# Optimization experiments

Measured on AMD Instinct MI355X. Metric: run time of the kernel, lower is better.

Reference implementation:

```python
import jax, jax.numpy as jnp
import numpy as np

N_ROWS = 262144
FEAT = 1024
N_CORES = 4096
SEG = N_ROWS // N_CORES
H1 = H2 = H3 = 1024
NUM_CLASSES = 2
BN_EPS = 1e-5


def setup_inputs() -> dict:
    key = jax.random.key(0)
    ks = jax.random.split(key, 12)
    x = jax.random.normal(ks[0], (N_ROWS, FEAT), dtype=jnp.float32)
    # equal-length segments: start indices 0, SEG, 2*SEG, ...
    corelen = (jnp.arange(N_CORES) * SEG).astype(jnp.int64)
    def lin(k, din, dout):
        kw, kb = jax.random.split(k)
        W = jax.random.normal(kw, (din, dout), dtype=jnp.float32) / np.sqrt(din)
        b = jnp.zeros((dout,), dtype=jnp.float32)
        return W, b
    W1, b1 = lin(ks[1], FEAT, H1)
    W2, b2 = lin(ks[2], H1, H2)
    W3, b3 = lin(ks[3], H2, H3)
    W4, b4 = lin(ks[4], H3, NUM_CLASSES)
    g1 = jnp.ones((H1,), jnp.float32); be1 = jnp.zeros((H1,), jnp.float32)
    g2 = jnp.ones((H2,), jnp.float32); be2 = jnp.zeros((H2,), jnp.float32)
    g3 = jnp.ones((H3,), jnp.float32); be3 = jnp.zeros((H3,), jnp.float32)
    return {"x": x, "corelen": corelen,
            "W1": W1, "b1": b1, "g1": g1, "be1": be1,
            "W2": W2, "b2": b2, "g2": g2, "be2": be2,
            "W3": W3, "b3": b3, "g3": g3, "be3": be3,
            "W4": W4, "b4": b4}


def _batchnorm(h, g, b):
    # BatchNorm1d, training mode: biased batch statistics over the batch dim
    m = jnp.mean(h, axis=0)
    v = jnp.mean(jnp.square(h - m), axis=0)
    return g * (h - m) * jax.lax.rsqrt(v + BN_EPS) + b


def reference(x, corelen, W1, b1, g1, be1, W2, b2, g2, be2, W3, b3, g3, be3, W4, b4):
    n = x.shape[0]
    # segment id of row r = number of starts <= r, minus 1 (rows before
    # corelen[0] get id -1 and are dropped, matching the torch loop)
    seg_ids = jnp.searchsorted(corelen, jnp.arange(n), side="right") - 1
    agg = jax.ops.segment_sum(x, seg_ids, num_segments=corelen.shape[0])  # [C, FEAT]
    h = jax.nn.relu(_batchnorm(agg @ W1 + b1, g1, be1))
    h = jax.nn.relu(_batchnorm(h @ W2 + b2, g2, be2))
    h = jax.nn.relu(_batchnorm(h @ W3 + b3, g3, be3))
    return h @ W4 + b4  # [C, NUM_CLASSES]
```

## Files before the change

### kernel.cpp

```cpp
#include <hip/hip_runtime.h>
#include <hip/hip_bf16.h>
#include <stdint.h>

#define N_ROWS 262144
#define FEAT 1024
#define N_CORES 4096
#define HDIM 1024
#define BN_EPS 1e-5f

typedef __attribute__((ext_vector_type(8))) short bf16x8;
typedef __attribute__((ext_vector_type(8))) unsigned short u16x8;
typedef __attribute__((ext_vector_type(4))) float f32x4;

__device__ __forceinline__ unsigned short f2bf(float f) {
  __hip_bfloat16 h = __float2bfloat16(f);
  return __builtin_bit_cast(unsigned short, h);
}
__device__ __forceinline__ float bf2f(unsigned short u) {
  unsigned int x = ((unsigned int)u) << 16;
  return __builtin_bit_cast(float, x);
}

__device__ __forceinline__ void gll16(const unsigned short* g, unsigned short* l) {
  __builtin_amdgcn_global_load_lds(
      (const __attribute__((address_space(1))) void*)g,
      (__attribute__((address_space(3))) void*)l, 16, 0, 0);
}

__global__ __launch_bounds__(256)
void k_segsum(const float* __restrict__ x, const int* __restrict__ corelen,
              unsigned short* __restrict__ aggb) {
  const int seg = blockIdx.x;
  const int t = threadIdx.x;
  const int start = corelen[seg];
  const int end = (seg + 1 < N_CORES) ? corelen[seg + 1] : N_ROWS;
  float4 a0 = make_float4(0.f, 0.f, 0.f, 0.f);
  float4 a1 = make_float4(0.f, 0.f, 0.f, 0.f);
  const float* xp = x + (size_t)start * FEAT + t * 4;
  int r = start;
  for (; r + 2 <= end; r += 2) {
    const float4 v0 = *(const float4*)xp;
    const float4 v1 = *(const float4*)(xp + FEAT);
    a0.x += v0.x; a0.y += v0.y; a0.z += v0.z; a0.w += v0.w;
    a1.x += v1.x; a1.y += v1.y; a1.z += v1.z; a1.w += v1.w;
    xp += 2 * FEAT;
  }
  if (r < end) {
    const float4 v0 = *(const float4*)xp;
    a0.x += v0.x; a0.y += v0.y; a0.z += v0.z; a0.w += v0.w;
  }
  a0.x += a1.x; a0.y += a1.y; a0.z += a1.z; a0.w += a1.w;
  ushort4 o;
  o.x = f2bf(a0.x); o.y = f2bf(a0.y); o.z = f2bf(a0.z); o.w = f2bf(a0.w);
  *(ushort4*)(aggb + (size_t)seg * FEAT + t * 4) = o;
}

__global__ __launch_bounds__(256)
void k_transpose_all(const float* __restrict__ W1, const float* __restrict__ W2,
                     const float* __restrict__ W3, unsigned short* __restrict__ Wt) {
  __shared__ unsigned short tile[32][33];
  const int l = blockIdx.z;
  const float* W = (l == 0) ? W1 : (l == 1) ? W2 : W3;
  unsigned short* Wo = Wt + (size_t)l * HDIM * HDIM;
  const int tx = threadIdx.x, ty = threadIdx.y;
  const int n0 = blockIdx.x * 32, k0 = blockIdx.y * 32;
#pragma unroll
  for (int i = 0; i < 4; ++i)
    tile[ty + 8 * i][tx] = f2bf(W[(size_t)(k0 + ty + 8 * i) * HDIM + n0 + tx]);
  __syncthreads();
#pragma unroll
  for (int i = 0; i < 4; ++i)
    Wo[(size_t)(n0 + ty + 8 * i) * HDIM + k0 + tx] = tile[tx][ty + 8 * i];
}

#define BM 128
#define BN 64
#define BK 64
#define NT (HDIM / BK)
__global__ __launch_bounds__(512)
void k_gemm_bt(const unsigned short* __restrict__ A,
               const unsigned short* __restrict__ Bt,
               const float* __restrict__ bias,
               unsigned short* __restrict__ C,
               float* __restrict__ sums, float* __restrict__ sumsq) {
  __shared__ unsigned short As[2][BM * BK];
  __shared__ unsigned short Bs[2][BN * BK];
  const int t = threadIdx.x;
  const int lane = t & 63;
  const int wv = t >> 6;
  const int tileM = blockIdx.x * BM;
  const int tileN = blockIdx.y * BN;
  const int wr = (wv >> 1) * 32;
  const int wc = (wv & 1) * 32;
  const int fr = lane & 15;
  const int kk = (lane >> 4) * 8;
  const int lr = lane >> 3;
  const int sc = ((lane & 7) * 8) ^ (lr << 3);

  const unsigned short* pA = A + (size_t)(tileM + wv * 8 + lr) * HDIM + sc;
  const unsigned short* pB = Bt + (size_t)(tileN + wv * 8 + lr) * HDIM + sc;

  f32x4 acc[2][2] = {};

#define STAGE(buf, k0)                                                     \
  do {                                                                     \
    gll16(pA + (k0), &As[buf][(wv * 8) * BK]);                             \
    gll16(pA + (k0) + 64 * HDIM, &As[buf][(64 + wv * 8) * BK]);            \
    gll16(pB + (k0), &Bs[buf][(wv * 8) * BK]);                             \
  } while (0)

  STAGE(0, 0);
  __syncthreads();
  for (int kt = 0; kt < NT; ++kt) {
    const int cur = kt & 1;
    if (kt < NT - 1) STAGE(cur ^ 1, (kt + 1) * BK);
#pragma unroll
    for (int ks = 0; ks < 2; ++ks) {
      const int pc = (ks * 32 + kk) ^ ((fr & 7) << 3);
      bf16x8 af[2], bfv[2];
#pragma unroll
      for (int m = 0; m < 2; ++m)
        af[m] = *(const bf16x8*)&As[cur][(wr + m * 16 + fr) * BK + pc];
#pragma unroll
      for (int n = 0; n < 2; ++n)
        bfv[n] = *(const bf16x8*)&Bs[cur][(wc + n * 16 + fr) * BK + pc];
#pragma unroll
      for (int m = 0; m < 2; ++m)
#pragma unroll
        for (int n = 0; n < 2; ++n)
          acc[m][n] = __builtin_amdgcn_mfma_f32_16x16x32_bf16(af[m], bfv[n], acc[m][n], 0, 0, 0);
    }
    __syncthreads();
  }
#undef STAGE

  const int cr = (lane >> 4) * 4;
  const int cc = lane & 15;
#pragma unroll
  for (int n = 0; n < 2; ++n) {
    const int col = tileN + wc + n * 16 + cc;
    const float bv = bias[col];
    float s = 0.f, s2 = 0.f;
#pragma unroll
    for (int m = 0; m < 2; ++m) {
      unsigned short* cp = C + (size_t)(tileM + wr + m * 16 + cr) * HDIM + col;
#pragma unroll
      for (int j = 0; j < 4; ++j) {
        const float h = acc[m][n][j] + bv;
        cp[(size_t)j * HDIM] = f2bf(h);
        s += h; s2 += h * h;
      }
    }
    s  += __shfl_xor(s, 16, 64);  s  += __shfl_xor(s, 32, 64);
    s2 += __shfl_xor(s2, 16, 64); s2 += __shfl_xor(s2, 32, 64);
    if ((lane >> 4) == 0) {
      atomicAdd(&sums[col], s);
      atomicAdd(&sumsq[col], s2);
    }
  }
}

__global__ __launch_bounds__(256)
void k_norm_relu(const unsigned short* __restrict__ Hb,
                 const float* __restrict__ sums, const float* __restrict__ sumsq,
                 const float* __restrict__ g, const float* __restrict__ be,
                 unsigned short* __restrict__ Ab) {
  const size_t i8 = ((size_t)blockIdx.x * 256 + threadIdx.x) * 8;
  const u16x8 v = *(const u16x8*)(Hb + i8);
  const int c = (int)(i8 & (HDIM - 1));
  u16x8 o;
#pragma unroll
  for (int j = 0; j < 8; ++j) {
    const float mean = sums[c + j] * (1.f / N_CORES);
    const float var = sumsq[c + j] * (1.f / N_CORES) - mean * mean;
    const float sc = g[c + j] * rsqrtf(var + BN_EPS);
    const float sh = be[c + j] - mean * sc;
    o[j] = f2bf(fmaxf(bf2f(v[j]) * sc + sh, 0.f));
  }
  *(u16x8*)(Ab + i8) = o;
}

__global__ __launch_bounds__(256)
void k_final(const unsigned short* __restrict__ Hb,
             const float* __restrict__ sums, const float* __restrict__ sumsq,
             const float* __restrict__ g, const float* __restrict__ be,
             const float* __restrict__ W4, const float* __restrict__ b4,
             float* __restrict__ out) {
  const int t = threadIdx.x;
  const int w = t >> 6, lane = t & 63;
  const int row = blockIdx.x * 4 + w;
  const int kbase = lane * 16;
  const unsigned short* a = Hb + (size_t)row * HDIM + kbase;
  float s0 = 0.f, s1 = 0.f;
#pragma unroll
  for (int j = 0; j < 16; ++j) {
    const int col = kbase + j;
    const float mean = sums[col] * (1.f / N_CORES);
    const float var = sumsq[col] * (1.f / N_CORES) - mean * mean;
    const float sc = g[col] * rsqrtf(var + BN_EPS);
    const float sh = be[col] - mean * sc;
    const float av = fmaxf(bf2f(a[j]) * sc + sh, 0.f);
    s0 += av * W4[col * 2 + 0];
    s1 += av * W4[col * 2 + 1];
  }
#pragma unroll
  for (int off = 32; off >= 1; off >>= 1) {
    s0 += __shfl_down(s0, off, 64);
    s1 += __shfl_down(s1, off, 64);
  }
  if (lane == 0) {
    out[row * 2 + 0] = s0 + b4[0];
    out[row * 2 + 1] = s1 + b4[1];
  }
}

extern "C" void kernel_launch(void* const* d_in, const int* in_sizes, int n_in,
                              void* d_out, int out_size, void* d_ws, size_t ws_size,
                              hipStream_t stream) {
  (void)in_sizes; (void)n_in; (void)out_size; (void)ws_size;
  const float* x       = (const float*)d_in[0];
  const int* corelen   = (const int*)d_in[1];
  const float* W1  = (const float*)d_in[2];
  const float* b1  = (const float*)d_in[3];
  const float* g1  = (const float*)d_in[4];
  const float* be1 = (const float*)d_in[5];
  const float* W2  = (const float*)d_in[6];
  const float* b2  = (const float*)d_in[7];
  const float* g2  = (const float*)d_in[8];
  const float* be2 = (const float*)d_in[9];
  const float* W3  = (const float*)d_in[10];
  const float* b3  = (const float*)d_in[11];
  const float* g3  = (const float*)d_in[12];
  const float* be3 = (const float*)d_in[13];
  const float* W4  = (const float*)d_in[14];
  const float* b4  = (const float*)d_in[15];
  float* out = (float*)d_out;

  char* ws = (char*)d_ws;
  unsigned short* Hb   = (unsigned short*)(ws);
  unsigned short* Abf  = (unsigned short*)(ws + (8u << 20));
  unsigned short* Wt   = (unsigned short*)(ws + (16u << 20));
  float* stats = (float*)(ws + (22u << 20));

  hipMemsetAsync(stats, 0, 6 * HDIM * sizeof(float), stream);
  k_transpose_all<<<dim3(32, 32, 3), dim3(32, 8), 0, stream>>>(W1, W2, W3, Wt);
  k_segsum<<<N_CORES, 256, 0, stream>>>(x, corelen, Abf);

  const float* bs[3]  = {b1, b2, b3};
  const float* gs[3]  = {g1, g2, g3};
  const float* bes[3] = {be1, be2, be3};
  for (int l = 0; l < 3; ++l) {
    float* sums  = stats + l * 2 * HDIM;
    float* sumsq = sums + HDIM;
    k_gemm_bt<<<dim3(N_CORES / BM, HDIM / BN), 512, 0, stream>>>(
        Abf, Wt + (size_t)l * HDIM * HDIM, bs[l], Hb, sums, sumsq);
    if (l < 2)
      k_norm_relu<<<(N_CORES * HDIM / 8) / 256, 256, 0, stream>>>(
          Hb, sums, sumsq, gs[l], bes[l], Abf);
    else
      k_final<<<N_CORES / 4, 256, 0, stream>>>(
          Hb, sums, sumsq, gs[l], bes[l], W4, b4, out);
  }
}
```

Measured before the change: 302.3 us.

## Use single-wave 64x64 GEMM blocks with larger per-wave tiles and barrier-free pipelining

The GEMM block shrinks from eight waves over a 128x64 tile to one wave over a 64x64 tile. Each wave now computes a 4x4 grid of MFMA fragments instead of 2x2, which raises register-level reuse of the LDS fragments. Because only one wave owns the LDS buffers, __syncthreads is replaced by explicit vmcnt/lgkmcnt waits, and global-to-LDS loads run two stages ahead. The grid doubles to 1024 blocks per layer. LDS traffic per MFMA drops, at the cost of more accumulator registers, lower per-block parallelism and reliance on hand-counted waitcnt values.

Measured after the change: 295.5 us. 1.02x faster.

```diff
diff --git a/kernel.cpp b/kernel.cpp
--- a/kernel.cpp
+++ b/kernel.cpp
@@ -73,11 +73,11 @@
     Wo[(size_t)(n0 + ty + 8 * i) * HDIM + k0 + tx] = tile[tx][ty + 8 * i];
 }
 
-#define BM 128
+#define BM 64
 #define BN 64
 #define BK 64
 #define NT (HDIM / BK)
-__global__ __launch_bounds__(512)
+__global__ __launch_bounds__(64)
 void k_gemm_bt(const unsigned short* __restrict__ A,
                const unsigned short* __restrict__ Bt,
                const float* __restrict__ bias,
@@ -85,65 +85,71 @@
                float* __restrict__ sums, float* __restrict__ sumsq) {
   __shared__ unsigned short As[2][BM * BK];
   __shared__ unsigned short Bs[2][BN * BK];
-  const int t = threadIdx.x;
-  const int lane = t & 63;
-  const int wv = t >> 6;
+  const int lane = threadIdx.x;
   const int tileM = blockIdx.x * BM;
   const int tileN = blockIdx.y * BN;
-  const int wr = (wv >> 1) * 32;
-  const int wc = (wv & 1) * 32;
   const int fr = lane & 15;
   const int kk = (lane >> 4) * 8;
   const int lr = lane >> 3;
   const int sc = ((lane & 7) * 8) ^ (lr << 3);
 
-  const unsigned short* pA = A + (size_t)(tileM + wv * 8 + lr) * HDIM + sc;
-  const unsigned short* pB = Bt + (size_t)(tileN + wv * 8 + lr) * HDIM + sc;
-
-  f32x4 acc[2][2] = {};
+  const unsigned short* pA = A + (size_t)(tileM + lr) * HDIM + sc;
+  const unsigned short* pB = Bt + (size_t)(tileN + lr) * HDIM + sc;
+
+  f32x4 acc[4][4] = {};
 
 #define STAGE(buf, k0)                                                     \
   do {                                                                     \
-    gll16(pA + (k0), &As[buf][(wv * 8) * BK]);                             \
-    gll16(pA + (k0) + 64 * HDIM, &As[buf][(64 + wv * 8) * BK]);            \
-    gll16(pB + (k0), &Bs[buf][(wv * 8) * BK]);                             \
+    _Pragma("unroll") for (int j = 0; j < 8; ++j)                          \
+        gll16(pA + (k0) + j * 8 * HDIM, &As[buf][(j * 8) * BK]);           \
+    _Pragma("unroll") for (int j = 0; j < 8; ++j)                          \
+        gll16(pB + (k0) + j * 8 * HDIM, &Bs[buf][(j * 8) * BK]);           \
   } while (0)
 
   STAGE(0, 0);
-  __syncthreads();
+  STAGE(1, BK);
   for (int kt = 0; kt < NT; ++kt) {
     const int cur = kt & 1;
-    if (kt < NT - 1) STAGE(cur ^ 1, (kt + 1) * BK);
+    if (kt < NT - 1)
+      asm volatile("s_waitcnt vmcnt(16)" ::: "memory");
+    else
+      asm volatile("s_waitcnt vmcnt(0)" ::: "memory");
+    __builtin_amdgcn_sched_barrier(0);
+    bf16x8 af[2][4], bfv[2][4];
 #pragma unroll
     for (int ks = 0; ks < 2; ++ks) {
       const int pc = (ks * 32 + kk) ^ ((fr & 7) << 3);
-      bf16x8 af[2], bfv[2];
-#pragma unroll
-      for (int m = 0; m < 2; ++m)
-        af[m] = *(const bf16x8*)&As[cur][(wr + m * 16 + fr) * BK + pc];
-#pragma unroll
-      for (int n = 0; n < 2; ++n)
-        bfv[n] = *(const bf16x8*)&Bs[cur][(wc + n * 16 + fr) * BK + pc];
-#pragma unroll
-      for (int m = 0; m < 2; ++m)
-#pragma unroll
-        for (int n = 0; n < 2; ++n)
-          acc[m][n] = __builtin_amdgcn_mfma_f32_16x16x32_bf16(af[m], bfv[n], acc[m][n], 0, 0, 0);
+#pragma unroll
+      for (int m = 0; m < 4; ++m)
+        af[ks][m] = *(const bf16x8*)&As[cur][(m * 16 + fr) * BK + pc];
+#pragma unroll
+      for (int n = 0; n < 4; ++n)
+        bfv[ks][n] = *(const bf16x8*)&Bs[cur][(n * 16 + fr) * BK + pc];
     }
-    __syncthreads();
+    asm volatile("s_waitcnt lgkmcnt(0)" ::: "memory");
+    __builtin_amdgcn_sched_barrier(0);
+    if (kt + 2 < NT) STAGE(cur, (kt + 2) * BK);
+#pragma unroll
+    for (int ks = 0; ks < 2; ++ks)
+#pragma unroll
+      for (int m = 0; m < 4; ++m)
+#pragma unroll
+        for (int n = 0; n < 4; ++n)
+          acc[m][n] = __builtin_amdgcn_mfma_f32_16x16x32_bf16(
+              af[ks][m], bfv[ks][n], acc[m][n], 0, 0, 0);
   }
 #undef STAGE
 
   const int cr = (lane >> 4) * 4;
   const int cc = lane & 15;
 #pragma unroll
-  for (int n = 0; n < 2; ++n) {
-    const int col = tileN + wc + n * 16 + cc;
+  for (int n = 0; n < 4; ++n) {
+    const int col = tileN + n * 16 + cc;
     const float bv = bias[col];
     float s = 0.f, s2 = 0.f;
 #pragma unroll
-    for (int m = 0; m < 2; ++m) {
-      unsigned short* cp = C + (size_t)(tileM + wr + m * 16 + cr) * HDIM + col;
+    for (int m = 0; m < 4; ++m) {
+      unsigned short* cp = C + (size_t)(tileM + m * 16 + cr) * HDIM + col;
 #pragma unroll
       for (int j = 0; j < 4; ++j) {
         const float h = acc[m][n][j] + bv;
@@ -252,7 +258,7 @@
   for (int l = 0; l < 3; ++l) {
     float* sums  = stats + l * 2 * HDIM;
     float* sumsq = sums + HDIM;
-    k_gemm_bt<<<dim3(N_CORES / BM, HDIM / BN), 512, 0, stream>>>(
+    k_gemm_bt<<<dim3(N_CORES / BM, HDIM / BN), 64, 0, stream>>>(
         Abf, Wt + (size_t)l * HDIM * HDIM, bs[l], Hb, sums, sumsq);
     if (l < 2)
       k_norm_relu<<<(N_CORES * HDIM / 8) / 256, 256, 0, stream>>>(
```
